# Optimization experiments

Measured on AMD Instinct MI355X. Metric: run time of the kernel, lower is better.

The kernel has to match this reference:

```python
import jax, jax.numpy as jnp
import numpy as np
from functools import partial

N_NODES = 50000
N_EDGES = 600000
N_FEAT = 128
HID = [128, 64, 32, 16]
N_GRAPHS = 64
N_CLASSES = 10


def gcn_conv(x, W, b, src, dst, n_nodes):
    # PyG GCNConv: h = x @ W; propagate with symmetric norm over A + I; add bias.
    h = x @ W  # [N, out]
    ones = jnp.ones((src.shape[0],), dtype=x.dtype)
    deg = jax.ops.segment_sum(ones, dst, num_segments=n_nodes) + 1.0  # self-loop
    dinv = jax.lax.rsqrt(deg)
    coef = dinv[src] * dinv[dst]  # [E]
    agg = jax.ops.segment_sum(h[src] * coef[:, None], dst, num_segments=n_nodes)
    agg = agg + h * (dinv * dinv)[:, None]  # self-loop contribution
    return agg + b


def global_mean_pool(x, batch, n_graphs):
    s = jax.ops.segment_sum(x, batch, num_segments=n_graphs)
    cnt = jax.ops.segment_sum(jnp.ones((x.shape[0],), x.dtype), batch, num_segments=n_graphs)
    return s / jnp.maximum(cnt, 1.0)[:, None]


def setup_inputs() -> dict:
    key = jax.random.key(0)
    ks = jax.random.split(key, 16)
    x = jax.random.normal(ks[0], (N_NODES, N_FEAT), dtype=jnp.float32)
    edge_index = jax.random.randint(ks[1], (2, N_EDGES), 0, N_NODES, dtype=jnp.int64)
    batch = jnp.sort(jax.random.randint(ks[2], (N_NODES,), 0, N_GRAPHS, dtype=jnp.int64))

    def glorot(k, fan_in, fan_out):
        s = float(np.sqrt(6.0 / (fan_in + fan_out)))
        return jax.random.uniform(k, (fan_in, fan_out), jnp.float32, -s, s)

    dims = [N_FEAT] + HID
    params = {}
    for i in range(4):
        params[f"W{i+1}"] = glorot(ks[3 + i], dims[i], dims[i + 1])
        params[f"b{i+1}"] = jnp.zeros((dims[i + 1],), jnp.float32)
    params["Wlin"] = glorot(ks[7], HID[-1], N_CLASSES)
    params["blin"] = jnp.zeros((N_CLASSES,), jnp.float32)
    return {"x": x, "edge_index": edge_index, "batch": batch, **params}


def reference(x, edge_index, batch, W1, b1, W2, b2, W3, b3, W4, b4, Wlin, blin):
    src, dst = edge_index[0], edge_index[1]
    n = x.shape[0]
    h = jax.nn.relu(gcn_conv(x, W1, b1, src, dst, n))
    h = jax.nn.relu(gcn_conv(h, W2, b2, src, dst, n))
    h = jax.nn.relu(gcn_conv(h, W3, b3, src, dst, n))
    h = jax.nn.relu(gcn_conv(h, W4, b4, src, dst, n))
    g = global_mean_pool(h, batch, N_GRAPHS)  # [G, 16]
    return g @ Wlin + blin
```

## Files before the change

kernel.cpp:

```cpp
#include <hip/hip_runtime.h>
#include <hip/hip_bf16.h>


#define N_GRAPHS 64
#define N_CLASSES 10

typedef short bf8_t __attribute__((ext_vector_type(8)));
typedef float f4_t  __attribute__((ext_vector_type(4)));

__device__ __forceinline__ float b2f(unsigned int u) {
  return __uint_as_float(u << 16);
}
__device__ __forceinline__ unsigned short f2b(float f) {
  unsigned int x = __float_as_uint(f);
  x += 0x7fffu + ((x >> 16) & 1u);
  return (unsigned short)(x >> 16);
}

__device__ __forceinline__ void block_detect(const unsigned int* __restrict__ xraw,
    const unsigned int* __restrict__ eraw, int* f32, int* i64) {
  __shared__ int c_bf, c_nz;
  if (threadIdx.x == 0) { c_bf = 0; c_nz = 0; }
  __syncthreads();
  unsigned int d = xraw[threadIdx.x & 255];
  int e = (int)(((d & 0xffffu) >> 7) & 0xff);
  if (e >= 100 && e <= 140) atomicAdd(&c_bf, 1);
  if (eraw && threadIdx.x < 64 && eraw[2 * threadIdx.x + 1] != 0u) atomicAdd(&c_nz, 1);
  __syncthreads();
  *f32 = (c_bf < 150) ? 1 : 0;
  if (i64) *i64 = (c_nz == 0) ? 1 : 0;
}

struct WPtrs { const void* p[10]; };
static constexpr int WSEG[10] = {16384, 128, 8192, 64, 2048, 32, 512, 16, 160, 10};
static constexpr int WTOTAL   = 27546;
static constexpr int WOFF[10] = {0, 16384, 16512, 24704, 24768, 26816, 26848, 27360, 27376, 27536};

__global__ __launch_bounds__(256) void cvt_we_kernel(
    const unsigned int* __restrict__ xraw, WPtrs wp, unsigned short* __restrict__ wc,
    const int* __restrict__ braw, int* __restrict__ b32,
    const int* __restrict__ eraw, int* __restrict__ deg, int* __restrict__ rank,
    int BW, int BB, int n, int E) {
  int f32, i64;
  block_detect(xraw, (const unsigned int*)eraw, &f32, &i64);
  const int bid = blockIdx.x;
  if (bid < BW) {
    int i = bid * 256 + threadIdx.x;
    if (i >= WTOTAL) return;
    int off = i, s = 0;
    #pragma unroll
    for (int t = 0; t < 10; ++t) {
      if (s == 0 && off >= WSEG[t]) { off -= WSEG[t]; } else if (s == 0) { s = t + 1; }
    }
    s -= 1;
    int soff = off;
    if ((s & 1) == 0 && s <= 6) {
      int KB, FOUT;
      if (s == 0)      { KB = 4; FOUT = 128; }
      else if (s == 2) { KB = 4; FOUT = 64; }
      else if (s == 4) { KB = 2; FOUT = 32; }
      else             { KB = 1; FOUT = 16; }
      int j = off & 7, l = (off >> 3) & 63, f = off >> 9;
      int ct = f / KB, kb = f - ct * KB;
      int k = kb * 32 + ((l >> 4) << 3) + j;
      int nn = ct * 16 + (l & 15);
      soff = k * FOUT + nn;
    }
    const void* p = wp.p[s];
    wc[WOFF[s] + off] = f32 ? f2b(((const float*)p)[soff])
                            : ((const unsigned short*)p)[soff];
  } else if (bid < BW + BB) {
    int i = (bid - BW) * 256 + threadIdx.x;
    if (i < n) b32[i] = i64 ? braw[2 * i] : braw[i];
  } else {
    int e = (bid - BW - BB) * 256 + threadIdx.x;
    if (e >= E) return;
    int d = i64 ? eraw[2 * (E + e)] : eraw[E + e];
    rank[e] = atomicAdd(&deg[d], 1);
  }
}

__global__ __launch_bounds__(256) void scan_kernel(const int* __restrict__ deg,
    int* __restrict__ row_ptr, float* __restrict__ dinv,
    unsigned long long* __restrict__ desc, int n) {
  __shared__ int ws[4];
  __shared__ int s_total;
  __shared__ unsigned int s_prev;
  const int b = blockIdx.x, tid = threadIdx.x, lane = tid & 63, wv = tid >> 6;
  const int i = b * 256 + tid;
  int v = (i < n) ? deg[i] : 0;
  int x = v;
  #pragma unroll
  for (int off = 1; off < 64; off <<= 1) {
    int y = __shfl_up(x, off, 64);
    if (lane >= off) x += y;
  }
  if (lane == 63) ws[wv] = x;
  __syncthreads();
  int wbase = 0;
  for (int w = 0; w < wv; ++w) wbase += ws[w];
  int incl = x + wbase;
  if (tid == 0) {
    int tot = ws[0] + ws[1] + ws[2] + ws[3];
    s_total = tot;
    unsigned long long st = (b == 0) ? (2ULL << 62) : (1ULL << 62);
    atomicExch(&desc[b], st | (unsigned long long)(unsigned int)tot);
    if (b == 0) s_prev = 0u;
  }
  __syncthreads();
  if (b > 0 && wv == 0) {
    unsigned int running = 0;
    int j = b - 1;
    while (true) {
      int idx = j - lane;
      unsigned long long d;
      if (idx >= 0) {
        do { d = atomicAdd(&desc[idx], 0ULL); } while ((d >> 62) == 0ULL);
      } else {
        d = (2ULL << 62);
      }
      unsigned long long ball = __ballot((d >> 62) == 2ULL);
      int fp = ball ? (__ffsll((unsigned long long)ball) - 1) : 64;
      unsigned int contrib = (lane <= fp) ? (unsigned int)(d & 0xffffffffULL) : 0u;
      #pragma unroll
      for (int o = 32; o; o >>= 1) contrib += __shfl_xor(contrib, o, 64);
      running += contrib;
      if (fp < 64) break;
      j -= 64;
    }
    if (lane == 0) {
      atomicExch(&desc[b], (2ULL << 62) |
                 (unsigned long long)(unsigned int)(running + (unsigned int)s_total));
      s_prev = running;
    }
  }
  __syncthreads();
  int tot = (int)s_prev + incl;
  if (i < n) {
    row_ptr[i + 1] = tot;
    dinv[i] = rsqrtf((float)v + 1.0f);
  }
  if (i == 0) row_ptr[0] = 0;
}

__global__ __launch_bounds__(256) void fill_gemm1_kernel(
    const int* __restrict__ eraw, const unsigned int* __restrict__ xraw,
    const int* __restrict__ row_ptr, const int* __restrict__ rank,
    const float* __restrict__ dinv, uint2* __restrict__ csr,
    const unsigned short* __restrict__ Wf, unsigned short* __restrict__ H,
    int BE, int n, int E) {
  int f32, i64;
  block_detect(xraw, (const unsigned int*)eraw, &f32, &i64);
  if (blockIdx.x < BE) {
    int e = blockIdx.x * 256 + threadIdx.x;
    if (e < E) {
      int s, d;
      if (i64) { s = eraw[2 * e]; d = eraw[2 * (E + e)]; }
      else     { s = eraw[e];     d = eraw[E + e]; }
      int pos = row_ptr[d] + rank[e];
      uint2 v;
      v.x = (unsigned int)s;
      v.y = __float_as_uint(dinv[s] * dinv[d]);
      csr[pos] = v;
    }
    return;
  }
  const int b2 = blockIdx.x - BE;
  const int l = threadIdx.x & 63;
  const int r16 = l & 15, quad = l >> 4;
  const int m0 = (b2 * 4 + (threadIdx.x >> 6)) * 32;
  if (m0 >= n) return;
  bf8_t afrag[2][4];
  #pragma unroll
  for (int mt = 0; mt < 2; ++mt) {
    int node = m0 + mt * 16 + r16;
    int nc = node < n ? node : n - 1;
    if (f32) {
      const float* xp = (const float*)xraw + (size_t)nc * 128 + quad * 8;
      #pragma unroll
      for (int kb = 0; kb < 4; ++kb) {
        const float4* p4 = (const float4*)(xp + kb * 32);
        float4 u0 = p4[0], u1 = p4[1];
        bf8_t a;
        a[0] = (short)f2b(u0.x); a[1] = (short)f2b(u0.y);
        a[2] = (short)f2b(u0.z); a[3] = (short)f2b(u0.w);
        a[4] = (short)f2b(u1.x); a[5] = (short)f2b(u1.y);
        a[6] = (short)f2b(u1.z); a[7] = (short)f2b(u1.w);
        afrag[mt][kb] = a;
      }
    } else {
      const unsigned short* xp = (const unsigned short*)xraw + (size_t)nc * 128 + quad * 8;
      #pragma unroll
      for (int kb = 0; kb < 4; ++kb)
        afrag[mt][kb] = *(const bf8_t*)(xp + kb * 32);
    }
  }
  #pragma unroll
  for (int ct = 0; ct < 8; ++ct) {
    bf8_t bfrag[4];
    #pragma unroll
    for (int kb = 0; kb < 4; ++kb)
      bfrag[kb] = *(const bf8_t*)(Wf + ((ct * 4 + kb) * 64 + l) * 8);
    #pragma unroll
    for (int mt = 0; mt < 2; ++mt) {
      f4_t acc = {0.f, 0.f, 0.f, 0.f};
      #pragma unroll
      for (int kb = 0; kb < 4; ++kb)
        acc = __builtin_amdgcn_mfma_f32_16x16x32_bf16(afrag[mt][kb], bfrag[kb], acc, 0, 0, 0);
      #pragma unroll
      for (int r = 0; r < 4; ++r) {
        int node = m0 + mt * 16 + quad * 4 + r;
        if (node < n)
          H[(size_t)node * 128 + ct * 16 + r16] = f2b(acc[r]);
      }
    }
  }
}

template<int DW> struct UVec { unsigned int d[DW]; };
template<int DW>
__device__ __forceinline__ UVec<DW> uload(const unsigned int* p) {
  UVec<DW> r;
  if constexpr (DW == 4) { uint4 v = *(const uint4*)p; r.d[0]=v.x; r.d[1]=v.y; r.d[2]=v.z; r.d[3]=v.w; }
  else if constexpr (DW == 2) { uint2 v = *(const uint2*)p; r.d[0]=v.x; r.d[1]=v.y; }
  else { r.d[0] = *p; }
  return r;
}
template<int DW>
__device__ __forceinline__ void ustore(unsigned int* p, const UVec<DW>& v) {
  if constexpr (DW == 4) { *(uint4*)p = make_uint4(v.d[0], v.d[1], v.d[2], v.d[3]); }
  else if constexpr (DW == 2) { *(uint2*)p = make_uint2(v.d[0], v.d[1]); }
  else { *p = v.d[0]; }
}

template<int FIN, int FOUT, int LPG>
__global__ __launch_bounds__(256) void aggemm_kernel(
    const unsigned short* __restrict__ Hin,
    const int* __restrict__ row_ptr, const uint2* __restrict__ csr,
    const float* __restrict__ dinv, const unsigned short* __restrict__ bias,
    const unsigned short* __restrict__ Wf, unsigned short* __restrict__ Hout, int n) {
  constexpr int DW  = FIN / LPG / 2;
  constexpr int NPB = 256 / LPG;
  constexpr int LD  = FIN + 8;
  constexpr int KB  = FIN / 32;
  constexpr int CT  = FOUT / 16;
  constexpr int MT  = NPB / 16;
  __shared__ unsigned short T[NPB * LD];
  const int r = threadIdx.x / LPG, l = threadIdx.x % LPG;
  const int node0 = blockIdx.x * NPB;
  const int g = node0 + r;
  const unsigned int* H2 = (const unsigned int*)Hin;
  UVec<DW> o;
  #pragma unroll
  for (int d = 0; d < DW; ++d) o.d[d] = 0u;
  if (g < n) {
    float di = dinv[g];
    float c0 = di * di;
    float a[2 * DW];
    UVec<DW> hv = uload<DW>(H2 + (size_t)g * (FIN / 2) + l * DW);
    #pragma unroll
    for (int d = 0; d < DW; ++d) {
      a[2*d]   = b2f(hv.d[d] & 0xffffu) * c0;
      a[2*d+1] = b2f(hv.d[d] >> 16) * c0;
    }
    const int e0 = row_ptr[g], e1 = row_ptr[g + 1];
    for (int base = e0; base < e1; base += LPG) {
      int cnt = e1 - base < LPG ? e1 - base : LPG;
      uint2 my = csr[(base + l < e1) ? (base + l) : (e1 - 1)];
      for (int j = 0; j < cnt; ++j) {
        int s = __shfl((int)my.x, j, LPG);
        float c = __uint_as_float(__shfl((int)my.y, j, LPG));
        UVec<DW> v = uload<DW>(H2 + (size_t)s * (FIN / 2) + l * DW);
        #pragma unroll
        for (int d = 0; d < DW; ++d) {
          a[2*d]   = fmaf(b2f(v.d[d] & 0xffffu), c, a[2*d]);
          a[2*d+1] = fmaf(b2f(v.d[d] >> 16), c, a[2*d+1]);
        }
      }
    }
    UVec<DW> bb = uload<DW>((const unsigned int*)bias + l * DW);
    #pragma unroll
    for (int d = 0; d < DW; ++d) {
      float lo = fmaxf(a[2*d]   + b2f(bb.d[d] & 0xffffu), 0.f);
      float hi = fmaxf(a[2*d+1] + b2f(bb.d[d] >> 16), 0.f);
      o.d[d] = (unsigned int)f2b(lo) | ((unsigned int)f2b(hi) << 16);
    }
  }
  ustore<DW>((unsigned int*)&T[r * LD + l * DW * 2], o);
  __syncthreads();
  const int w = threadIdx.x >> 6;
  if (w < MT * CT && node0 < n) {
    const int mt = w / CT, ct = w % CT;
    const int ll = threadIdx.x & 63;
    const int r16 = ll & 15, quad = ll >> 4;
    bf8_t afrag[KB], bfrag[KB];
    #pragma unroll
    for (int kb = 0; kb < KB; ++kb) {
      afrag[kb] = *(const bf8_t*)(&T[(mt * 16 + r16) * LD + quad * 8 + kb * 32]);
      bfrag[kb] = *(const bf8_t*)(Wf + ((ct * KB + kb) * 64 + ll) * 8);
    }
    f4_t acc = {0.f, 0.f, 0.f, 0.f};
    #pragma unroll
    for (int kb = 0; kb < KB; ++kb)
      acc = __builtin_amdgcn_mfma_f32_16x16x32_bf16(afrag[kb], bfrag[kb], acc, 0, 0, 0);
    #pragma unroll
    for (int rr = 0; rr < 4; ++rr) {
      int node = node0 + mt * 16 + quad * 4 + rr;
      if (node < n)
        Hout[(size_t)node * FOUT + ct * 16 + r16] = f2b(acc[rr]);
    }
  }
}

__global__ __launch_bounds__(256) void agg_pool_kernel(
    const unsigned short* __restrict__ Hin,
    const int* __restrict__ row_ptr, const uint2* __restrict__ csr,
    const float* __restrict__ dinv, const unsigned short* __restrict__ bias,
    const int* __restrict__ batch, float* __restrict__ pooled,
    float* __restrict__ cnt, int n) {
  __shared__ float acc[N_GRAPHS * 16];
  __shared__ float ccnt[N_GRAPHS];
  for (int i = threadIdx.x; i < N_GRAPHS * 16; i += 256) acc[i] = 0.f;
  if (threadIdx.x < N_GRAPHS) ccnt[threadIdx.x] = 0.f;
  __syncthreads();
  const int r = threadIdx.x >> 3, l = threadIdx.x & 7;
  const int g = blockIdx.x * 32 + r;
  if (g < n) {
    const unsigned int* H2 = (const unsigned int*)Hin;
    float di = dinv[g];
    float c0 = di * di;
    unsigned int hv = H2[(size_t)g * 8 + l];
    float a0 = b2f(hv & 0xffffu) * c0;
    float a1 = b2f(hv >> 16) * c0;
    const int e0 = row_ptr[g], e1 = row_ptr[g + 1];
    for (int base = e0; base < e1; base += 8) {
      int cnt2 = e1 - base < 8 ? e1 - base : 8;
      uint2 my = csr[(base + l < e1) ? (base + l) : (e1 - 1)];
      for (int j = 0; j < cnt2; ++j) {
        int s = __shfl((int)my.x, j, 8);
        float c = __uint_as_float(__shfl((int)my.y, j, 8));
        unsigned int v = H2[(size_t)s * 8 + l];
        a0 = fmaf(b2f(v & 0xffffu), c, a0);
        a1 = fmaf(b2f(v >> 16), c, a1);
      }
    }
    unsigned int bb = ((const unsigned int*)bias)[l];
    a0 = fmaxf(a0 + b2f(bb & 0xffffu), 0.f);
    a1 = fmaxf(a1 + b2f(bb >> 16), 0.f);
    int gb = batch[g];
    atomicAdd(&acc[gb * 16 + l * 2 + 0], a0);
    atomicAdd(&acc[gb * 16 + l * 2 + 1], a1);
    if (l == 0) atomicAdd(&ccnt[gb], 1.f);
  }
  __syncthreads();
  for (int i = threadIdx.x; i < N_GRAPHS * 16; i += 256)
    if (acc[i] != 0.f) atomicAdd(&pooled[i], acc[i]);
  if (threadIdx.x < N_GRAPHS && ccnt[threadIdx.x] != 0.f)
    atomicAdd(&cnt[threadIdx.x], ccnt[threadIdx.x]);
}

__global__ __launch_bounds__(256) void final_kernel(const float* __restrict__ pooled,
    const float* __restrict__ cnt, const unsigned short* __restrict__ wc,
    void* __restrict__ out, const unsigned int* __restrict__ xraw) {
  int f32;
  block_detect(xraw, nullptr, &f32, nullptr);
  int id = blockIdx.x * 256 + threadIdx.x;
  if (id >= N_GRAPHS * N_CLASSES) return;
  const unsigned short* Wlin = wc + WOFF[8];
  const unsigned short* blin = wc + WOFF[9];
  int g = id / N_CLASSES, c = id - g * N_CLASSES;
  float inv = 1.0f / fmaxf(cnt[g], 1.0f);
  float a = b2f(blin[c]);
  #pragma unroll
  for (int f = 0; f < 16; ++f)
    a = fmaf(pooled[g * 16 + f] * inv, b2f(Wlin[f * N_CLASSES + c]), a);
  if (f32) ((float*)out)[id] = a;
  else     ((unsigned short*)out)[id] = f2b(a);
}

extern "C" void kernel_launch(void* const* d_in, const int* in_sizes, int n_in,
                              void* d_out, int out_size, void* d_ws, size_t ws_size,
                              hipStream_t stream) {
  const unsigned int* xraw = (const unsigned int*)d_in[0];
  const int* eraw          = (const int*)d_in[1];
  const int* braw          = (const int*)d_in[2];

  const int N = in_sizes[2];
  const int E = in_sizes[1] / 2;
  const int nb = (N + 255) / 256;

  char* p = (char*)d_ws;
  auto alloc = [&](size_t bytes) -> void* {
    void* r = (void*)p;
    p += (bytes + 255) & ~(size_t)255;
    return r;
  };
  const size_t off_desc = ((size_t)N * 4 + 255) & ~(size_t)255;
  const size_t off_pool = (off_desc + (size_t)nb * 8 + 255) & ~(size_t)255;
  const size_t ztotal   = off_pool + (N_GRAPHS * 16 + N_GRAPHS) * 4;
  char* zbase = (char*)alloc(ztotal);
  int*   deg    = (int*)zbase;
  unsigned long long* desc = (unsigned long long*)(zbase + off_desc);
  float* pooled = (float*)(zbase + off_pool);
  float* cntf   = pooled + N_GRAPHS * 16;

  int*   row_ptr  = (int*)  alloc((size_t)(N + 1) * 4);
  int*   rank     = (int*)  alloc((size_t)E * 4);
  float* dinv     = (float*)alloc((size_t)N * 4);
  int*   batch32  = (int*)  alloc((size_t)N * 4);
  uint2* csr      = (uint2*)alloc((size_t)E * 8);
  unsigned short* wcan  = (unsigned short*)alloc((size_t)WTOTAL * 2);
  unsigned short* hbufA = (unsigned short*)alloc((size_t)N * 128 * 2);
  unsigned short* hbufB = (unsigned short*)alloc((size_t)N * 128 * 2);

  hipMemsetAsync(zbase, 0, ztotal, stream);

  WPtrs wp;
  for (int i = 0; i < 10; ++i) wp.p[i] = d_in[3 + i];

  const int BW = (WTOTAL + 255) / 256;
  const int BB = nb;
  const int BE = (E + 255) / 256;
  cvt_we_kernel<<<BW + BB + BE, 256, 0, stream>>>(xraw, wp, wcan, braw, batch32,
      eraw, deg, rank, BW, BB, N, E);

  scan_kernel<<<nb, 256, 0, stream>>>(deg, row_ptr, dinv, desc, N);

  const unsigned short* W1 = wcan + WOFF[0];
  const unsigned short* b1 = wcan + WOFF[1];
  const unsigned short* W2 = wcan + WOFF[2];
  const unsigned short* b2 = wcan + WOFF[3];
  const unsigned short* W3 = wcan + WOFF[4];
  const unsigned short* b3 = wcan + WOFF[5];
  const unsigned short* W4 = wcan + WOFF[6];
  const unsigned short* b4 = wcan + WOFF[7];

  const int G1 = (N + 127) / 128;
  fill_gemm1_kernel<<<BE + G1, 256, 0, stream>>>(eraw, xraw, row_ptr, rank, dinv,
      csr, W1, hbufA, BE, N, E);

  aggemm_kernel<128, 64, 16><<<(N + 15) / 16, 256, 0, stream>>>(
      hbufA, row_ptr, csr, dinv, b1, W2, hbufB, N);
  aggemm_kernel<64, 32, 8><<<(N + 31) / 32, 256, 0, stream>>>(
      hbufB, row_ptr, csr, dinv, b2, W3, hbufA, N);
  aggemm_kernel<32, 16, 8><<<(N + 31) / 32, 256, 0, stream>>>(
      hbufA, row_ptr, csr, dinv, b3, W4, hbufB, N);
  agg_pool_kernel<<<(N + 31) / 32, 256, 0, stream>>>(hbufB, row_ptr, csr, dinv, b4,
      batch32, pooled, cntf, N);

  final_kernel<<<(N_GRAPHS * N_CLASSES + 255) / 256, 256, 0, stream>>>(pooled, cntf, wcan, d_out, xraw);
}
```

Before: 227.5 us.

## Move layer-1 GEMM into first kernel with LDS-staged W1 and padded degree counters

The layer-1 feature GEMM moves from the fill kernel into the first preprocessing kernel, so it runs alongside weight conversion and degree counting. Each GEMM block converts and swizzles W1 from the raw input into 32 KB of shared memory instead of reading the pre-swizzled global copy. The per-node degree counters are spaced 64 bytes apart, which should reduce atomic contention and false sharing on shared cache lines. In exchange, every GEMM block redoes the W1 conversion, the large shared-memory allocation may cut occupancy for the other block types in that kernel, and the degree buffer and its memset grow sixteenfold.

```diff
diff --git a/kernel.cpp b/kernel.cpp
--- a/kernel.cpp
+++ b/kernel.cpp
@@ -36,16 +36,82 @@
 static constexpr int WTOTAL   = 27546;
 static constexpr int WOFF[10] = {0, 16384, 16512, 24704, 24768, 26816, 26848, 27360, 27376, 27536};
 
-__global__ __launch_bounds__(256) void cvt_we_kernel(
+__global__ __launch_bounds__(256) void cvtwe_gemm1_kernel(
     const unsigned int* __restrict__ xraw, WPtrs wp, unsigned short* __restrict__ wc,
     const int* __restrict__ braw, int* __restrict__ b32,
     const int* __restrict__ eraw, int* __restrict__ deg, int* __restrict__ rank,
-    int BW, int BB, int n, int E) {
+    unsigned short* __restrict__ H,
+    int G1, int BW, int BB, int n, int E) {
+  __shared__ unsigned short Wlds[16384];
   int f32, i64;
   block_detect(xraw, (const unsigned int*)eraw, &f32, &i64);
   const int bid = blockIdx.x;
-  if (bid < BW) {
-    int i = bid * 256 + threadIdx.x;
+  if (bid < G1) {
+    const void* w1 = wp.p[0];
+    #pragma unroll 4
+    for (int it = 0; it < 64; ++it) {
+      int srcI = it * 256 + threadIdx.x;
+      int k = srcI >> 7, nn = srcI & 127;
+      int kb = k >> 5, j = k & 7, quad = (k >> 3) & 3;
+      int ct = nn >> 4, r16c = nn & 15;
+      int l = quad * 16 + r16c;
+      int f = ct * 4 + kb;
+      unsigned short w = f32 ? f2b(((const float*)w1)[srcI])
+                             : ((const unsigned short*)w1)[srcI];
+      Wlds[(f * 64 + l) * 8 + j] = w;
+    }
+    __syncthreads();
+    const int l = threadIdx.x & 63;
+    const int r16 = l & 15, quad = l >> 4;
+    const int m0 = (bid * 4 + (threadIdx.x >> 6)) * 32;
+    if (m0 >= n) return;
+    bf8_t afrag[2][4];
+    #pragma unroll
+    for (int mt = 0; mt < 2; ++mt) {
+      int node = m0 + mt * 16 + r16;
+      int nc = node < n ? node : n - 1;
+      if (f32) {
+        const float* xp = (const float*)xraw + (size_t)nc * 128 + quad * 8;
+        #pragma unroll
+        for (int kb = 0; kb < 4; ++kb) {
+          const float4* p4 = (const float4*)(xp + kb * 32);
+          float4 u0 = p4[0], u1 = p4[1];
+          bf8_t a;
+          a[0] = (short)f2b(u0.x); a[1] = (short)f2b(u0.y);
+          a[2] = (short)f2b(u0.z); a[3] = (short)f2b(u0.w);
+          a[4] = (short)f2b(u1.x); a[5] = (short)f2b(u1.y);
+          a[6] = (short)f2b(u1.z); a[7] = (short)f2b(u1.w);
+          afrag[mt][kb] = a;
+        }
+      } else {
+        const unsigned short* xp = (const unsigned short*)xraw + (size_t)nc * 128 + quad * 8;
+        #pragma unroll
+        for (int kb = 0; kb < 4; ++kb)
+          afrag[mt][kb] = *(const bf8_t*)(xp + kb * 32);
+      }
+    }
+    #pragma unroll
+    for (int ct = 0; ct < 8; ++ct) {
+      bf8_t bfrag[4];
+      #pragma unroll
+      for (int kb = 0; kb < 4; ++kb)
+        bfrag[kb] = *(const bf8_t*)(&Wlds[((ct * 4 + kb) * 64 + l) * 8]);
+      #pragma unroll
+      for (int mt = 0; mt < 2; ++mt) {
+        f4_t acc = {0.f, 0.f, 0.f, 0.f};
+        #pragma unroll
+        for (int kb = 0; kb < 4; ++kb)
+          acc = __builtin_amdgcn_mfma_f32_16x16x32_bf16(afrag[mt][kb], bfrag[kb], acc, 0, 0, 0);
+        #pragma unroll
+        for (int r = 0; r < 4; ++r) {
+          int node = m0 + mt * 16 + quad * 4 + r;
+          if (node < n)
+            H[(size_t)node * 128 + ct * 16 + r16] = f2b(acc[r]);
+        }
+      }
+    }
+  } else if (bid < G1 + BW) {
+    int i = (bid - G1) * 256 + threadIdx.x;
     if (i >= WTOTAL) return;
     int off = i, s = 0;
     #pragma unroll
@@ -69,14 +135,14 @@
     const void* p = wp.p[s];
     wc[WOFF[s] + off] = f32 ? f2b(((const float*)p)[soff])
                             : ((const unsigned short*)p)[soff];
-  } else if (bid < BW + BB) {
-    int i = (bid - BW) * 256 + threadIdx.x;
+  } else if (bid < G1 + BW + BB) {
+    int i = (bid - G1 - BW) * 256 + threadIdx.x;
     if (i < n) b32[i] = i64 ? braw[2 * i] : braw[i];
   } else {
-    int e = (bid - BW - BB) * 256 + threadIdx.x;
+    int e = (bid - G1 - BW - BB) * 256 + threadIdx.x;
     if (e >= E) return;
     int d = i64 ? eraw[2 * (E + e)] : eraw[E + e];
-    rank[e] = atomicAdd(&deg[d], 1);
+    rank[e] = atomicAdd(&deg[(size_t)d << 4], 1);
   }
 }
 
@@ -88,7 +154,7 @@
   __shared__ unsigned int s_prev;
   const int b = blockIdx.x, tid = threadIdx.x, lane = tid & 63, wv = tid >> 6;
   const int i = b * 256 + tid;
-  int v = (i < n) ? deg[i] : 0;
+  int v = (i < n) ? deg[(size_t)i << 4] : 0;
   int x = v;
   #pragma unroll
   for (int off = 1; off < 64; off <<= 1) {
@@ -143,78 +209,22 @@
   if (i == 0) row_ptr[0] = 0;
 }
 
-__global__ __launch_bounds__(256) void fill_gemm1_kernel(
+__global__ __launch_bounds__(256) void fill_kernel(
     const int* __restrict__ eraw, const unsigned int* __restrict__ xraw,
     const int* __restrict__ row_ptr, const int* __restrict__ rank,
-    const float* __restrict__ dinv, uint2* __restrict__ csr,
-    const unsigned short* __restrict__ Wf, unsigned short* __restrict__ H,
-    int BE, int n, int E) {
+    const float* __restrict__ dinv, uint2* __restrict__ csr, int E) {
   int f32, i64;
   block_detect(xraw, (const unsigned int*)eraw, &f32, &i64);
-  if (blockIdx.x < BE) {
-    int e = blockIdx.x * 256 + threadIdx.x;
-    if (e < E) {
-      int s, d;
-      if (i64) { s = eraw[2 * e]; d = eraw[2 * (E + e)]; }
-      else     { s = eraw[e];     d = eraw[E + e]; }
-      int pos = row_ptr[d] + rank[e];
-      uint2 v;
-      v.x = (unsigned int)s;
-      v.y = __float_as_uint(dinv[s] * dinv[d]);
-      csr[pos] = v;
-    }
-    return;
-  }
-  const int b2 = blockIdx.x - BE;
-  const int l = threadIdx.x & 63;
-  const int r16 = l & 15, quad = l >> 4;
-  const int m0 = (b2 * 4 + (threadIdx.x >> 6)) * 32;
-  if (m0 >= n) return;
-  bf8_t afrag[2][4];
-  #pragma unroll
-  for (int mt = 0; mt < 2; ++mt) {
-    int node = m0 + mt * 16 + r16;
-    int nc = node < n ? node : n - 1;
-    if (f32) {
-      const float* xp = (const float*)xraw + (size_t)nc * 128 + quad * 8;
-      #pragma unroll
-      for (int kb = 0; kb < 4; ++kb) {
-        const float4* p4 = (const float4*)(xp + kb * 32);
-        float4 u0 = p4[0], u1 = p4[1];
-        bf8_t a;
-        a[0] = (short)f2b(u0.x); a[1] = (short)f2b(u0.y);
-        a[2] = (short)f2b(u0.z); a[3] = (short)f2b(u0.w);
-        a[4] = (short)f2b(u1.x); a[5] = (short)f2b(u1.y);
-        a[6] = (short)f2b(u1.z); a[7] = (short)f2b(u1.w);
-        afrag[mt][kb] = a;
-      }
-    } else {
-      const unsigned short* xp = (const unsigned short*)xraw + (size_t)nc * 128 + quad * 8;
-      #pragma unroll
-      for (int kb = 0; kb < 4; ++kb)
-        afrag[mt][kb] = *(const bf8_t*)(xp + kb * 32);
-    }
-  }
-  #pragma unroll
-  for (int ct = 0; ct < 8; ++ct) {
-    bf8_t bfrag[4];
-    #pragma unroll
-    for (int kb = 0; kb < 4; ++kb)
-      bfrag[kb] = *(const bf8_t*)(Wf + ((ct * 4 + kb) * 64 + l) * 8);
-    #pragma unroll
-    for (int mt = 0; mt < 2; ++mt) {
-      f4_t acc = {0.f, 0.f, 0.f, 0.f};
-      #pragma unroll
-      for (int kb = 0; kb < 4; ++kb)
-        acc = __builtin_amdgcn_mfma_f32_16x16x32_bf16(afrag[mt][kb], bfrag[kb], acc, 0, 0, 0);
-      #pragma unroll
-      for (int r = 0; r < 4; ++r) {
-        int node = m0 + mt * 16 + quad * 4 + r;
-        if (node < n)
-          H[(size_t)node * 128 + ct * 16 + r16] = f2b(acc[r]);
-      }
-    }
-  }
+  int e = blockIdx.x * 256 + threadIdx.x;
+  if (e >= E) return;
+  int s, d;
+  if (i64) { s = eraw[2 * e]; d = eraw[2 * (E + e)]; }
+  else     { s = eraw[e];     d = eraw[E + e]; }
+  int pos = row_ptr[d] + rank[e];
+  uint2 v;
+  v.x = (unsigned int)s;
+  v.y = __float_as_uint(dinv[s] * dinv[d]);
+  csr[pos] = v;
 }
 
 template<int DW> struct UVec { unsigned int d[DW]; };
@@ -395,7 +405,7 @@
     p += (bytes + 255) & ~(size_t)255;
     return r;
   };
-  const size_t off_desc = ((size_t)N * 4 + 255) & ~(size_t)255;
+  const size_t off_desc = ((size_t)N * 64 + 255) & ~(size_t)255;
   const size_t off_pool = (off_desc + (size_t)nb * 8 + 255) & ~(size_t)255;
   const size_t ztotal   = off_pool + (N_GRAPHS * 16 + N_GRAPHS) * 4;
   char* zbase = (char*)alloc(ztotal);
@@ -421,12 +431,12 @@
   const int BW = (WTOTAL + 255) / 256;
   const int BB = nb;
   const int BE = (E + 255) / 256;
-  cvt_we_kernel<<<BW + BB + BE, 256, 0, stream>>>(xraw, wp, wcan, braw, batch32,
-      eraw, deg, rank, BW, BB, N, E);
+  const int G1 = (N + 127) / 128;
+  cvtwe_gemm1_kernel<<<G1 + BW + BB + BE, 256, 0, stream>>>(xraw, wp, wcan,
+      braw, batch32, eraw, deg, rank, hbufA, G1, BW, BB, N, E);
 
   scan_kernel<<<nb, 256, 0, stream>>>(deg, row_ptr, dinv, desc, N);
 
-  const unsigned short* W1 = wcan + WOFF[0];
   const unsigned short* b1 = wcan + WOFF[1];
   const unsigned short* W2 = wcan + WOFF[2];
   const unsigned short* b2 = wcan + WOFF[3];
@@ -435,9 +445,7 @@
   const unsigned short* W4 = wcan + WOFF[6];
   const unsigned short* b4 = wcan + WOFF[7];
 
-  const int G1 = (N + 127) / 128;
-  fill_gemm1_kernel<<<BE + G1, 256, 0, stream>>>(eraw, xraw, row_ptr, rank, dinv,
-      csr, W1, hbufA, BE, N, E);
+  fill_kernel<<<BE, 256, 0, stream>>>(eraw, xraw, row_ptr, rank, dinv, csr, E);
 
   aggemm_kernel<128, 64, 16><<<(N + 15) / 16, 256, 0, stream>>>(
       hbufA, row_ptr, csr, dinv, b1, W2, hbufB, N);
```

New measurement: 226.8 us. No clear change (-0.3%).
